# Kernel optimization log

Measured on AMD Instinct MI355X. Metric: run time of the kernel, lower is better.

## Reference

```python
import jax, jax.numpy as jnp
import numpy as np
import math

B, S, HID, H = 1, 512, 256, 8
D = HID // H
SCALE = 1.0 / math.sqrt(D)
PI = math.pi


def setup_inputs() -> dict:
    key = jax.random.key(0)
    ks = jax.random.split(key, 6)
    x = jax.random.normal(ks[0], (B, S, HID), dtype=jnp.float32)
    w = lambda k: jax.random.normal(k, (HID, HID), dtype=jnp.float32) * 0.02
    return {
        'x': x,
        'wq': w(ks[1]), 'bq': jnp.zeros((HID,), jnp.float32),
        'wk': w(ks[2]), 'bk': jnp.zeros((HID,), jnp.float32),
        'wv': w(ks[3]), 'bv': jnp.zeros((HID,), jnp.float32),
        'wo': w(ks[4]), 'bo': jnp.zeros((HID,), jnp.float32),
    }


def _split_heads(t):
    # [B,S,HID] -> [B,H,S,D]
    return t.reshape(B, S, H, D).transpose(0, 2, 1, 3)


def reference(x, wq, bq, wk, bk, wv, bv, wo, bo):
    # Linear projections (torch nn.Linear: x @ W.T + b)
    q = _split_heads(x @ wq.T + bq)
    k = _split_heads(x @ wk.T + bk)
    v = _split_heads(x @ wv.T + bv)

    omega = jax.nn.sigmoid(q) * PI      # [B,H,S,D]
    amplitude = jax.nn.sigmoid(k)       # [B,H,S,D]
    phase = jnp.tanh(v) * PI            # [B,H,S,D]

    # relative position i-j, [S,S]
    pos = (jnp.arange(S)[:, None] - jnp.arange(S)[None, :]).astype(jnp.float32)
    # wave interference tensor [B,H,S,D,S] (query i, dim d, key j)
    interaction = amplitude[..., None] * jnp.cos(
        omega[..., None] * pos[None, None, :, None, :] + phase[..., None])
    patterns = jax.nn.softmax(interaction * SCALE, axis=-1)  # softmax over keys j
    # contract over key positions: per-dim attention
    context = jnp.einsum('bhidj,bhjd->bhid', patterns, v)    # [B,H,S,D]
    context = context.transpose(0, 2, 1, 3).reshape(B, S, HID)
    return context @ wo.T + bo
```

## Files before the change

### kernel.cpp

```cpp
#include <hip/hip_runtime.h>
#include <math.h>

#define SEQ 512
#define HID 256
#define NH 8
#define DH 32
#define PI_F 3.14159265358979323846f
#define SCALE_F 0.17677669529663687f
#define LOG2E_F 1.4426950408889634f

#define OFF_OMEGA 0
#define OFF_AMP   131072
#define OFF_PHASE 262144
#define OFF_V     393216
#define OFF_CTX   524288
#define OFF_PQKV  655360
#define OFF_POUT  2228224

__global__ __launch_bounds__(256) void gemm_slice(
    const float* __restrict__ A,
    const float* __restrict__ W0, const float* __restrict__ W1,
    const float* __restrict__ W2, float* __restrict__ part)
{
    const int which = blockIdx.y;
    const float* W = (which == 0) ? W0 : (which == 1) ? W1 : W2;
    const int bx = blockIdx.x;
    const int ks = bx & 3;
    const int ct = (bx >> 2) & 3;
    const int rt = bx >> 4;
    const int r0 = rt * 64, c0 = ct * 64, k0 = ks * 64;

    __shared__ float xs[64 * 68];
    __shared__ float wts[64 * 64];

    const int tid = threadIdx.x;
#pragma unroll
    for (int it = 0; it < 4; it++) {
        int idx = tid + it * 256;
        int rr = idx >> 4, f4 = idx & 15;
        float4 av = *(const float4*)(A + (r0 + rr) * HID + k0 + 4 * f4);
        *(float4*)&xs[rr * 68 + 4 * f4] = av;
        float4 wv = *(const float4*)(W + (c0 + rr) * HID + k0 + 4 * f4);
        int cw = rr ^ ((f4 & 7) << 2);
        wts[(4 * f4 + 0) * 64 + cw] = wv.x;
        wts[(4 * f4 + 1) * 64 + cw] = wv.y;
        wts[(4 * f4 + 2) * 64 + cw] = wv.z;
        wts[(4 * f4 + 3) * 64 + cw] = wv.w;
    }
    __syncthreads();

    const int rg = tid >> 4, cg = tid & 15;
    float acc[4][4];
#pragma unroll
    for (int i = 0; i < 4; i++)
#pragma unroll
        for (int j = 0; j < 4; j++) acc[i][j] = 0.f;

#pragma unroll
    for (int g = 0; g < 16; g++) {
        float xfa[4][4], wfa[4][4];
#pragma unroll
        for (int i = 0; i < 4; i++) {
            float4 xv = *(const float4*)&xs[(4 * rg + i) * 68 + 4 * g];
            xfa[i][0] = xv.x; xfa[i][1] = xv.y; xfa[i][2] = xv.z; xfa[i][3] = xv.w;
        }
        const int sw = (g & 7) << 2;
#pragma unroll
        for (int m = 0; m < 4; m++) {
            float4 wv = *(const float4*)&wts[(4 * g + m) * 64 + ((4 * cg) ^ sw)];
            wfa[m][0] = wv.x; wfa[m][1] = wv.y; wfa[m][2] = wv.z; wfa[m][3] = wv.w;
        }
#pragma unroll
        for (int m = 0; m < 4; m++)
#pragma unroll
            for (int i = 0; i < 4; i++)
#pragma unroll
                for (int j = 0; j < 4; j++)
                    acc[i][j] = fmaf(xfa[i][m], wfa[m][j], acc[i][j]);
    }

    float* P = part + (size_t)(which * 4 + ks) * (SEQ * HID);
#pragma unroll
    for (int i = 0; i < 4; i++) {
        float4 o;
        o.x = acc[i][0]; o.y = acc[i][1]; o.z = acc[i][2]; o.w = acc[i][3];
        *(float4*)&P[(r0 + 4 * rg + i) * HID + c0 + 4 * cg] = o;
    }
}

__global__ __launch_bounds__(256) void reduce_qkv(
    const float* __restrict__ part,
    const float* __restrict__ bq, const float* __restrict__ bk,
    const float* __restrict__ bv, float* __restrict__ ws)
{
    const int which = blockIdx.y;
    const int r = blockIdx.x, c = threadIdx.x;
    const float* P = part + (size_t)which * 4 * (SEQ * HID) + r * HID + c;
    float s = (P[0] + P[SEQ * HID]) + (P[2 * SEQ * HID] + P[3 * SEQ * HID]);
    const int o = r * HID + c;
    if (which == 0) {
        s += bq[c];
        ws[OFF_OMEGA + o] = PI_F / (1.f + expf(-s));
    } else if (which == 1) {
        s += bk[c];
        ws[OFF_AMP + o] = 1.f / (1.f + expf(-s));
    } else {
        s += bv[c];
        ws[OFF_V + o] = s;
        ws[OFF_PHASE + o] = PI_F * tanhf(s);
    }
}

__global__ __launch_bounds__(256) void reduce_out(
    const float* __restrict__ part, const float* __restrict__ bo,
    float* __restrict__ out)
{
    const int r = blockIdx.x, c = threadIdx.x;
    const float* P = part + r * HID + c;
    float s = (P[0] + P[SEQ * HID]) + (P[2 * SEQ * HID] + P[3 * SEQ * HID]);
    out[r * HID + c] = s + bo[c];
}

__global__ __launch_bounds__(256) void wave_attn(const float* __restrict__ ws,
                                                 float* __restrict__ ctx)
{
    const int h  = blockIdx.y;
    const int il = threadIdx.x >> 5;
    const int d  = threadIdx.x & 31;
    const int i  = blockIdx.x * 8 + il;
    const int col = h * DH + d;

    const float w  = ws[OFF_OMEGA + i * HID + col];
    const float aL = ws[OFF_AMP + i * HID + col] * (SCALE_F * LOG2E_F);
    const float ph = ws[OFF_PHASE + i * HID + col];
    const float* vcol = ws + OFF_V + col;

    float sw_, cw;
    sincosf(w, &sw_, &cw);
    float c2 = cw * cw - sw_ * sw_, s2 = 2.f * sw_ * cw;
    float c4 = c2 * c2 - s2 * s2,   s4 = 2.f * s2 * c2;

    float th0 = fmaf(w, (float)i, ph);
    float s0, cc0;
    sincosf(th0, &s0, &cc0);

    float pc[4], psn[4];
    pc[0] = cc0; psn[0] = s0;
#pragma unroll
    for (int k = 1; k < 4; k++) {
        float nc = pc[k - 1] * cw + psn[k - 1] * sw_;
        float ns = psn[k - 1] * cw - pc[k - 1] * sw_;
        pc[k] = nc; psn[k] = ns;
    }
    float p[4], q[4], den[4], num[4];
#pragma unroll
    for (int k = 0; k < 4; k++) {
        p[k] = aL * pc[k]; q[k] = aL * psn[k];
        den[k] = 0.f; num[k] = 0.f;
    }

#pragma unroll 4
    for (int t = 0; t < SEQ / 4; t++) {
        float v0 = vcol[(4 * t + 0) * HID];
        float v1 = vcol[(4 * t + 1) * HID];
        float v2v = vcol[(4 * t + 2) * HID];
        float v3 = vcol[(4 * t + 3) * HID];
        float e0 = __builtin_amdgcn_exp2f(p[0]);
        float e1 = __builtin_amdgcn_exp2f(p[1]);
        float e2 = __builtin_amdgcn_exp2f(p[2]);
        float e3 = __builtin_amdgcn_exp2f(p[3]);
        den[0] += e0; den[1] += e1; den[2] += e2; den[3] += e3;
        num[0] = fmaf(e0, v0, num[0]);
        num[1] = fmaf(e1, v1, num[1]);
        num[2] = fmaf(e2, v2v, num[2]);
        num[3] = fmaf(e3, v3, num[3]);
#pragma unroll
        for (int k = 0; k < 4; k++) {
            float np = p[k] * c4 + q[k] * s4;
            float nq = q[k] * c4 - p[k] * s4;
            p[k] = np; q[k] = nq;
        }
    }
    float denom = (den[0] + den[1]) + (den[2] + den[3]);
    float numer = (num[0] + num[1]) + (num[2] + num[3]);
    ctx[i * HID + col] = numer / denom;
}

extern "C" void kernel_launch(void* const* d_in, const int* in_sizes, int n_in,
                              void* d_out, int out_size, void* d_ws, size_t ws_size,
                              hipStream_t stream) {
    const float* x  = (const float*)d_in[0];
    const float* wq = (const float*)d_in[1];
    const float* bq = (const float*)d_in[2];
    const float* wk = (const float*)d_in[3];
    const float* bk = (const float*)d_in[4];
    const float* wv = (const float*)d_in[5];
    const float* bv = (const float*)d_in[6];
    const float* wo = (const float*)d_in[7];
    const float* bo = (const float*)d_in[8];

    float* ws = (float*)d_ws;

    hipLaunchKernelGGL(gemm_slice, dim3(128, 3), dim3(256), 0, stream,
                       x, wq, wk, wv, ws + OFF_PQKV);
    hipLaunchKernelGGL(reduce_qkv, dim3(SEQ, 3), dim3(256), 0, stream,
                       ws + OFF_PQKV, bq, bk, bv, ws);
    hipLaunchKernelGGL(wave_attn, dim3(SEQ / 8, NH), dim3(256), 0, stream,
                       ws, ws + OFF_CTX);
    hipLaunchKernelGGL(gemm_slice, dim3(128, 1), dim3(256), 0, stream,
                       ws + OFF_CTX, wo, wo, wo, ws + OFF_POUT);
    hipLaunchKernelGGL(reduce_out, dim3(SEQ), dim3(256), 0, stream,
                       ws + OFF_POUT, bo, (float*)d_out);
}
```

Baseline: 107.4 us.

## Drop split-K partials and fuse bias/activation epilogues into GEMM kernels

The QKV and output projections no longer split K into four slices that write partial sums to workspace. Each block now loops over the full K dimension and applies bias plus sigmoid/tanh (or bias alone) directly in its epilogue. This removes two reduction kernel launches and the partial-sum traffic through global memory. The cost is fewer blocks (96 and 32 instead of 384 and 128), so each GEMM has less parallelism and a longer serial K loop per block.

```diff
diff --git a/kernel.cpp b/kernel.cpp
--- a/kernel.cpp
+++ b/kernel.cpp
@@ -14,111 +14,131 @@
 #define OFF_PHASE 262144
 #define OFF_V     393216
 #define OFF_CTX   524288
-#define OFF_PQKV  655360
-#define OFF_POUT  2228224
-
-__global__ __launch_bounds__(256) void gemm_slice(
-    const float* __restrict__ A,
-    const float* __restrict__ W0, const float* __restrict__ W1,
-    const float* __restrict__ W2, float* __restrict__ part)
+
+__device__ __forceinline__ void gemm_tile(
+    const float* __restrict__ A, const float* __restrict__ W,
+    int r0, int c0, int tid, float (&acc)[4][4],
+    float* __restrict__ xs, float* __restrict__ wts)
+{
+#pragma unroll
+    for (int i = 0; i < 4; i++)
+#pragma unroll
+        for (int j = 0; j < 4; j++) acc[i][j] = 0.f;
+
+    const int rg = tid >> 4, cg = tid & 15;
+
+    for (int k0 = 0; k0 < HID; k0 += 64) {
+#pragma unroll
+        for (int it = 0; it < 4; it++) {
+            int idx = tid + it * 256;
+            int rr = idx >> 4, f4 = idx & 15;
+            float4 av = *(const float4*)(A + (r0 + rr) * HID + k0 + 4 * f4);
+            *(float4*)&xs[rr * 68 + 4 * f4] = av;
+            float4 wv = *(const float4*)(W + (c0 + rr) * HID + k0 + 4 * f4);
+            int cw = rr ^ ((f4 & 7) << 2);
+            wts[(4 * f4 + 0) * 64 + cw] = wv.x;
+            wts[(4 * f4 + 1) * 64 + cw] = wv.y;
+            wts[(4 * f4 + 2) * 64 + cw] = wv.z;
+            wts[(4 * f4 + 3) * 64 + cw] = wv.w;
+        }
+        __syncthreads();
+#pragma unroll
+        for (int g = 0; g < 16; g++) {
+            float xfa[4][4], wfa[4][4];
+#pragma unroll
+            for (int i = 0; i < 4; i++) {
+                float4 xv = *(const float4*)&xs[(4 * rg + i) * 68 + 4 * g];
+                xfa[i][0] = xv.x; xfa[i][1] = xv.y; xfa[i][2] = xv.z; xfa[i][3] = xv.w;
+            }
+            const int sw = (g & 7) << 2;
+#pragma unroll
+            for (int m = 0; m < 4; m++) {
+                float4 wv = *(const float4*)&wts[(4 * g + m) * 64 + ((4 * cg) ^ sw)];
+                wfa[m][0] = wv.x; wfa[m][1] = wv.y; wfa[m][2] = wv.z; wfa[m][3] = wv.w;
+            }
+#pragma unroll
+            for (int m = 0; m < 4; m++)
+#pragma unroll
+                for (int i = 0; i < 4; i++)
+#pragma unroll
+                    for (int j = 0; j < 4; j++)
+                        acc[i][j] = fmaf(xfa[i][m], wfa[m][j], acc[i][j]);
+        }
+        __syncthreads();
+    }
+}
+
+__global__ __launch_bounds__(256) void gemm_qkv_act(
+    const float* __restrict__ x,
+    const float* __restrict__ wq, const float* __restrict__ bq,
+    const float* __restrict__ wk, const float* __restrict__ bk,
+    const float* __restrict__ wv, const float* __restrict__ bv,
+    float* __restrict__ ws)
 {
     const int which = blockIdx.y;
-    const float* W = (which == 0) ? W0 : (which == 1) ? W1 : W2;
-    const int bx = blockIdx.x;
-    const int ks = bx & 3;
-    const int ct = (bx >> 2) & 3;
-    const int rt = bx >> 4;
-    const int r0 = rt * 64, c0 = ct * 64, k0 = ks * 64;
+    const float* W = (which == 0) ? wq : (which == 1) ? wk : wv;
+    const float* B = (which == 0) ? bq : (which == 1) ? bk : bv;
+    const int ct = blockIdx.x & 3;
+    const int rt = blockIdx.x >> 2;
+    const int r0 = rt * 64, c0 = ct * 64;
 
     __shared__ float xs[64 * 68];
     __shared__ float wts[64 * 64];
 
     const int tid = threadIdx.x;
-#pragma unroll
-    for (int it = 0; it < 4; it++) {
-        int idx = tid + it * 256;
-        int rr = idx >> 4, f4 = idx & 15;
-        float4 av = *(const float4*)(A + (r0 + rr) * HID + k0 + 4 * f4);
-        *(float4*)&xs[rr * 68 + 4 * f4] = av;
-        float4 wv = *(const float4*)(W + (c0 + rr) * HID + k0 + 4 * f4);
-        int cw = rr ^ ((f4 & 7) << 2);
-        wts[(4 * f4 + 0) * 64 + cw] = wv.x;
-        wts[(4 * f4 + 1) * 64 + cw] = wv.y;
-        wts[(4 * f4 + 2) * 64 + cw] = wv.z;
-        wts[(4 * f4 + 3) * 64 + cw] = wv.w;
-    }
-    __syncthreads();
+    float acc[4][4];
+    gemm_tile(x, W, r0, c0, tid, acc, xs, wts);
 
     const int rg = tid >> 4, cg = tid & 15;
+    float4 b4 = *(const float4*)(B + c0 + 4 * cg);
+    float bb[4] = {b4.x, b4.y, b4.z, b4.w};
+
+#pragma unroll
+    for (int i = 0; i < 4; i++) {
+        int row = r0 + 4 * rg + i;
+#pragma unroll
+        for (int j = 0; j < 4; j++) {
+            float val = acc[i][j] + bb[j];
+            int o = row * HID + c0 + 4 * cg + j;
+            if (which == 0) {
+                ws[OFF_OMEGA + o] = PI_F / (1.f + expf(-val));
+            } else if (which == 1) {
+                ws[OFF_AMP + o] = 1.f / (1.f + expf(-val));
+            } else {
+                ws[OFF_V + o] = val;
+                ws[OFF_PHASE + o] = PI_F * tanhf(val);
+            }
+        }
+    }
+}
+
+__global__ __launch_bounds__(256) void gemm_out(
+    const float* __restrict__ ctx, const float* __restrict__ wo,
+    const float* __restrict__ bo, float* __restrict__ out)
+{
+    const int ct = blockIdx.x & 3;
+    const int rt = blockIdx.x >> 2;
+    const int r0 = rt * 64, c0 = ct * 64;
+
+    __shared__ float xs[64 * 68];
+    __shared__ float wts[64 * 64];
+
+    const int tid = threadIdx.x;
     float acc[4][4];
-#pragma unroll
-    for (int i = 0; i < 4; i++)
-#pragma unroll
-        for (int j = 0; j < 4; j++) acc[i][j] = 0.f;
-
-#pragma unroll
-    for (int g = 0; g < 16; g++) {
-        float xfa[4][4], wfa[4][4];
-#pragma unroll
-        for (int i = 0; i < 4; i++) {
-            float4 xv = *(const float4*)&xs[(4 * rg + i) * 68 + 4 * g];
-            xfa[i][0] = xv.x; xfa[i][1] = xv.y; xfa[i][2] = xv.z; xfa[i][3] = xv.w;
-        }
-        const int sw = (g & 7) << 2;
-#pragma unroll
-        for (int m = 0; m < 4; m++) {
-            float4 wv = *(const float4*)&wts[(4 * g + m) * 64 + ((4 * cg) ^ sw)];
-            wfa[m][0] = wv.x; wfa[m][1] = wv.y; wfa[m][2] = wv.z; wfa[m][3] = wv.w;
-        }
-#pragma unroll
-        for (int m = 0; m < 4; m++)
-#pragma unroll
-            for (int i = 0; i < 4; i++)
-#pragma unroll
-                for (int j = 0; j < 4; j++)
-                    acc[i][j] = fmaf(xfa[i][m], wfa[m][j], acc[i][j]);
-    }
-
-    float* P = part + (size_t)(which * 4 + ks) * (SEQ * HID);
+    gemm_tile(ctx, wo, r0, c0, tid, acc, xs, wts);
+
+    const int rg = tid >> 4, cg = tid & 15;
+    float4 b4 = *(const float4*)(bo + c0 + 4 * cg);
 #pragma unroll
     for (int i = 0; i < 4; i++) {
+        int row = r0 + 4 * rg + i;
         float4 o;
-        o.x = acc[i][0]; o.y = acc[i][1]; o.z = acc[i][2]; o.w = acc[i][3];
-        *(float4*)&P[(r0 + 4 * rg + i) * HID + c0 + 4 * cg] = o;
-    }
-}
-
-__global__ __launch_bounds__(256) void reduce_qkv(
-    const float* __restrict__ part,
-    const float* __restrict__ bq, const float* __restrict__ bk,
-    const float* __restrict__ bv, float* __restrict__ ws)
-{
-    const int which = blockIdx.y;
-    const int r = blockIdx.x, c = threadIdx.x;
-    const float* P = part + (size_t)which * 4 * (SEQ * HID) + r * HID + c;
-    float s = (P[0] + P[SEQ * HID]) + (P[2 * SEQ * HID] + P[3 * SEQ * HID]);
-    const int o = r * HID + c;
-    if (which == 0) {
-        s += bq[c];
-        ws[OFF_OMEGA + o] = PI_F / (1.f + expf(-s));
-    } else if (which == 1) {
-        s += bk[c];
-        ws[OFF_AMP + o] = 1.f / (1.f + expf(-s));
-    } else {
-        s += bv[c];
-        ws[OFF_V + o] = s;
-        ws[OFF_PHASE + o] = PI_F * tanhf(s);
-    }
-}
-
-__global__ __launch_bounds__(256) void reduce_out(
-    const float* __restrict__ part, const float* __restrict__ bo,
-    float* __restrict__ out)
-{
-    const int r = blockIdx.x, c = threadIdx.x;
-    const float* P = part + r * HID + c;
-    float s = (P[0] + P[SEQ * HID]) + (P[2 * SEQ * HID] + P[3 * SEQ * HID]);
-    out[r * HID + c] = s + bo[c];
+        o.x = acc[i][0] + b4.x;
+        o.y = acc[i][1] + b4.y;
+        o.z = acc[i][2] + b4.z;
+        o.w = acc[i][3] + b4.w;
+        *(float4*)&out[row * HID + c0 + 4 * cg] = o;
+    }
 }
 
 __global__ __launch_bounds__(256) void wave_attn(const float* __restrict__ ws,
@@ -201,14 +221,10 @@
 
     float* ws = (float*)d_ws;
 
-    hipLaunchKernelGGL(gemm_slice, dim3(128, 3), dim3(256), 0, stream,
-                       x, wq, wk, wv, ws + OFF_PQKV);
-    hipLaunchKernelGGL(reduce_qkv, dim3(SEQ, 3), dim3(256), 0, stream,
-                       ws + OFF_PQKV, bq, bk, bv, ws);
+    hipLaunchKernelGGL(gemm_qkv_act, dim3(32, 3), dim3(256), 0, stream,
+                       x, wq, bq, wk, bk, wv, bv, ws);
     hipLaunchKernelGGL(wave_attn, dim3(SEQ / 8, NH), dim3(256), 0, stream,
                        ws, ws + OFF_CTX);
-    hipLaunchKernelGGL(gemm_slice, dim3(128, 1), dim3(256), 0, stream,
-                       ws + OFF_CTX, wo, wo, wo, ws + OFF_POUT);
-    hipLaunchKernelGGL(reduce_out, dim3(SEQ), dim3(256), 0, stream,
-                       ws + OFF_POUT, bo, (float*)d_out);
-}
+    hipLaunchKernelGGL(gemm_out, dim3(32), dim3(256), 0, stream,
+                       ws + OFF_CTX, wo, bo, (float*)d_out);
+}
```

Result: slower. 116.1 us (+8.1%).
